# Kernel tuning notes

Measured on AMD Instinct MI355X. Metric: run time of the kernel, lower is better.

The kernel has to match this reference:

```python
import jax, jax.numpy as jnp
import numpy as np

B, C, H, W = 4, 512, 64, 64
CQ = C // 8


def setup_inputs() -> dict:
    key = jax.random.key(0)
    ks = jax.random.split(key, 8)
    s = 0.05
    return {
        "x": jax.random.normal(ks[0], (B, C, H, W), dtype=jnp.float32),
        "wq": jax.random.normal(ks[1], (CQ, C), dtype=jnp.float32) * s,
        "bq": jax.random.normal(ks[2], (CQ,), dtype=jnp.float32) * s,
        "wk": jax.random.normal(ks[3], (CQ, C), dtype=jnp.float32) * s,
        "bk": jax.random.normal(ks[4], (CQ,), dtype=jnp.float32) * s,
        "wv": jax.random.normal(ks[5], (C, C), dtype=jnp.float32) * s,
        "bv": jax.random.normal(ks[6], (C,), dtype=jnp.float32) * s,
        "gamma": jax.random.normal(ks[7], (1,), dtype=jnp.float32) * 0.1,
    }


def reference(x, wq, bq, wk, bk, wv, bv, gamma):
    b, c, h, w = x.shape
    f = x.reshape(b, c, h * w)                       # [B, C, N]
    # 1x1 Conv1d == per-position matmul + bias
    q = jnp.einsum("dc,bcn->bdn", wq, f) + bq[:, None]   # [B, C/8, N]
    k = jnp.einsum("dc,bcn->bdn", wk, f) + bk[:, None]   # [B, C/8, N]
    v = jnp.einsum("dc,bcn->bdn", wv, f) + bv[:, None]   # [B, C, N]
    # query_key[b, i, j] = q_i . k_j  ; softmax over axis=1 (query index)
    qk = jnp.einsum("bdi,bdj->bij", q, k)                # [B, N, N]
    attn = jax.nn.softmax(qk, axis=1)
    o = jnp.einsum("bci,bij->bcj", v, attn)              # [B, C, N]
    return gamma * o.reshape(b, c, h, w) + x
```

## Files before the change

kernel.cpp:

```cpp
#include <hip/hip_runtime.h>
#include <hip/hip_bf16.h>

#define NB 4
#define NC 512
#define NN 4096
#define NM 640
#define IB 64
#define NT (NN / IB)
#define LOG2E 1.4426950408889634f

typedef __attribute__((ext_vector_type(8))) short bf16x8;
typedef __attribute__((ext_vector_type(4))) float f32x4;

__device__ __forceinline__ f32x4 mfma16(bf16x8 a, bf16x8 b, f32x4 c) {
  return __builtin_amdgcn_mfma_f32_16x16x32_bf16(a, b, c, 0, 0, 0);
}

__device__ __forceinline__ unsigned short f2bf(float f) {
  unsigned int u = __float_as_uint(f);
  u += 0x7fffu + ((u >> 16) & 1u);
  return (unsigned short)(u >> 16);
}

typedef const __attribute__((address_space(1))) char gchar_t;
typedef __attribute__((address_space(3))) char lchar_t;

__global__ void pack_w(const float* __restrict__ wq, const float* __restrict__ bq,
                       const float* __restrict__ wk, const float* __restrict__ bk,
                       const float* __restrict__ wv, const float* __restrict__ bv,
                       unsigned short* __restrict__ W, float* __restrict__ bias) {
  int idx = blockIdx.x * 256 + threadIdx.x;
  if (idx < NM * NC) {
    int r = idx >> 9, c = idx & (NC - 1);
    float v;
    if (r < 64) v = wq[r * NC + c];
    else if (r < 128) v = wk[(r - 64) * NC + c];
    else v = wv[(r - 128) * NC + c];
    W[idx] = f2bf(v);
  }
  if (idx < NM)
    bias[idx] = (idx < 64) ? bq[idx] : (idx < 128 ? bk[idx - 64] : bv[idx - 128]);
}

__global__ void xpose(const float* __restrict__ x, unsigned short* __restrict__ XT) {
  __shared__ float t[64][65];
  int b = blockIdx.z;
  int c0 = blockIdx.y * 64, n0 = blockIdx.x * 64;
  int tid = threadIdx.x;
  int lr = tid >> 4;
  int lc4 = (tid & 15) * 4;
  const float* xb = x + (size_t)b * NC * NN;
#pragma unroll
  for (int i = 0; i < 4; ++i) {
    int c = i * 16 + lr;
    float4 v = *reinterpret_cast<const float4*>(xb + (size_t)(c0 + c) * NN + n0 + lc4);
    t[c][lc4 + 0] = v.x; t[c][lc4 + 1] = v.y; t[c][lc4 + 2] = v.z; t[c][lc4 + 3] = v.w;
  }
  __syncthreads();
  unsigned short* xtb = XT + (size_t)b * NN * NC;
#pragma unroll
  for (int i = 0; i < 4; ++i) {
    int n = i * 16 + lr;
    union { unsigned short h[4]; unsigned long long u; } pk;
#pragma unroll
    for (int e = 0; e < 4; ++e) pk.h[e] = f2bf(t[lc4 + e][n]);
    *reinterpret_cast<unsigned long long*>(xtb + (size_t)(n0 + n) * NC + c0 + lc4) = pk.u;
  }
}

__global__ __launch_bounds__(512) void gemm_qkv(
    const unsigned short* __restrict__ W, const float* __restrict__ bias,
    const unsigned short* __restrict__ XT,
    unsigned short* __restrict__ QT, unsigned short* __restrict__ KT,
    unsigned short* __restrict__ V) {
  int b = blockIdx.z;
  int m0 = blockIdx.y * 80;
  int wave = threadIdx.x >> 6, lane = threadIdx.x & 63;
  int nw = blockIdx.x * 512 + wave * 64;
  int lcol = lane & 15, lkg = lane >> 4;
  const unsigned short* xtb = XT + (size_t)b * NN * NC;
  f32x4 acc[5][4] = {};
  for (int k0 = 0; k0 < NC; k0 += 32) {
    int ko = k0 + lkg * 8;
    bf16x8 afr[5], bfr[4];
#pragma unroll
    for (int i = 0; i < 5; ++i)
      afr[i] = *reinterpret_cast<const bf16x8*>(W + (size_t)(m0 + 16 * i + lcol) * NC + ko);
#pragma unroll
    for (int j = 0; j < 4; ++j)
      bfr[j] = *reinterpret_cast<const bf16x8*>(xtb + (size_t)(nw + 16 * j + lcol) * NC + ko);
#pragma unroll
    for (int i = 0; i < 5; ++i)
#pragma unroll
      for (int j = 0; j < 4; ++j)
        acc[i][j] = mfma16(afr[i], bfr[j], acc[i][j]);
  }
  int rbase = lkg * 4;
#pragma unroll
  for (int i = 0; i < 5; ++i) {
    int mrow = m0 + 16 * i;
    if (mrow < 128) {
      bool isq = mrow < 64;
      unsigned short* T = isq ? (QT + (size_t)b * NN * 64) : (KT + (size_t)b * NN * 64);
      int mb = mrow & 63;
      float sc = isq ? LOG2E : 1.0f;
#pragma unroll
      for (int j = 0; j < 4; ++j) {
        int n = nw + 16 * j + lcol;
        union { unsigned short h[4]; unsigned long long u; } pk;
#pragma unroll
        for (int r = 0; r < 4; ++r)
          pk.h[r] = f2bf((acc[i][j][r] + bias[mrow + rbase + r]) * sc);
        *reinterpret_cast<unsigned long long*>(T + (size_t)n * 64 + mb + rbase) = pk.u;
      }
    } else {
      unsigned short* vb = V + (size_t)b * NC * NN;
#pragma unroll
      for (int r = 0; r < 4; ++r) {
        int m = mrow + rbase + r;
        float bs = bias[m];
        int c = m - 128;
#pragma unroll
        for (int j = 0; j < 4; ++j) {
          int n = nw + 16 * j + lcol;
          vb[(size_t)c * NN + n] = f2bf(acc[i][j][r] + bs);
        }
      }
    }
  }
}

__global__ __launch_bounds__(512, 2) void attn_pv(
    const unsigned short* __restrict__ QT, const unsigned short* __restrict__ KT,
    const unsigned short* __restrict__ V, const float* __restrict__ x,
    const float* __restrict__ gamma, float* __restrict__ out) {
  int bid = blockIdx.x;
  int b = (bid & 7) >> 1;
  int jb = ((bid >> 3) << 1) | (bid & 1);
  int j0 = jb * 64;
  int wave = threadIdx.x >> 6, lane = threadIdx.x & 63;
  int lcol = lane & 15, lkg = lane >> 4;
  int sw = wave >> 1;
  int fnh = wave & 1;

  __shared__ __align__(16) unsigned short vlds[2][512 * IB];
  __shared__ __align__(16) unsigned short plds[2][64 * IB];
  __shared__ float sml[4][16][4];

  const unsigned short* qt = QT + (size_t)b * NN * 64;
  const unsigned short* kt = KT + (size_t)b * NN * 64;
  const unsigned short* vp = V + (size_t)b * NC * NN;

  const int lrow = lane >> 3;
  const int lswz = ((lane & 7) ^ lrow) << 3;
  lchar_t* vbase = (lchar_t*)vlds;

  auto stage = [&](int itv, int buf) {
    int i0 = (itv & (NT - 1)) * IB;
    lchar_t* lb = vbase + (size_t)buf * (512 * IB * 2) + wave * (64 * IB * 2);
#pragma unroll
    for (int q = 0; q < 8; ++q) {
      const unsigned short* gp = vp + (size_t)(wave * 64 + q * 8 + lrow) * NN + i0 + lswz;
      __builtin_amdgcn_global_load_lds((gchar_t*)gp, lb + q * 1024, 16, 0, 0);
    }
  };

  bf16x8 kfr[2][2];
#pragma unroll
  for (int f = 0; f < 2; ++f) {
    int fn = 2 * fnh + f;
#pragma unroll
    for (int ks = 0; ks < 2; ++ks)
      kfr[f][ks] = *reinterpret_cast<const bf16x8*>(
          kt + (size_t)(j0 + 16 * fn + lcol) * 64 + ks * 32 + lkg * 8);
  }

  f32x4 oacc[4][4] = {};
  float l_loc[2] = {0.f, 0.f};

  const int jw0 = 16 * (2 * fnh) + lcol, jw1 = jw0 + 16;
  const int pwoff0 = (jw0 * 128 + sw * 32 + lkg * 8) ^ ((jw0 & 7) << 4);
  const int pwoff1 = (jw1 * 128 + sw * 32 + lkg * 8) ^ ((jw1 & 7) << 4);
  const int pxm = (lcol & 7) << 4;
  const int pk0 = lcol * 128 + ((lkg * 16) ^ (pxm & 0x30)) + (pxm & 0x40);
  const int pk1 = pk0 ^ 64;
  const int vk0 = wave * 8192 + lcol * 128 + ((lkg ^ (lcol & 7)) * 16);
  const int vk1 = vk0 ^ 64;

  const char* Pb[2] = {(const char*)plds, (const char*)plds + 64 * IB * 2};
  const char* Vbs[2] = {(const char*)vlds, (const char*)vlds + 512 * IB * 2};

  stage(0, 0);
  bf16x8 qA[2], qB[2];
  {
    int row = sw * 16 + lcol;
    qA[0] = *reinterpret_cast<const bf16x8*>(qt + (size_t)row * 64 + lkg * 8);
    qA[1] = *reinterpret_cast<const bf16x8*>(qt + (size_t)row * 64 + 32 + lkg * 8);
  }

#define PV_ITER(IT, QC, QN, BUF)                                                  \
  {                                                                               \
    const int it_ = (IT);                                                         \
    stage(it_ + 1, (BUF) ^ 1);                                                    \
    f32x4 s[2] = {};                                                              \
    _Pragma("unroll") for (int ks = 0; ks < 2; ++ks)                              \
      _Pragma("unroll") for (int f = 0; f < 2; ++f)                               \
        s[f] = mfma16(QC[ks], kfr[f][ks], s[f]);                                  \
    {                                                                             \
      int row = ((it_ + 1) & (NT - 1)) * IB + sw * 16 + lcol;                     \
      QN[0] = *reinterpret_cast<const bf16x8*>(qt + (size_t)row * 64 + lkg * 8);  \
      QN[1] = *reinterpret_cast<const bf16x8*>(qt + (size_t)row * 64 + 32 + lkg * 8); \
    }                                                                             \
    char* pb = (char*)Pb[BUF];                                                    \
    {                                                                             \
      float p0 = exp2f(s[0][0]), p1 = exp2f(s[0][1]);                             \
      float p2 = exp2f(s[0][2]), p3 = exp2f(s[0][3]);                             \
      l_loc[0] += (p0 + p1) + (p2 + p3);                                          \
      union { unsigned short h[4]; unsigned long long u; } pk;                    \
      pk.h[0] = f2bf(p0); pk.h[1] = f2bf(p1);                                     \
      pk.h[2] = f2bf(p2); pk.h[3] = f2bf(p3);                                     \
      *reinterpret_cast<unsigned long long*>(pb + pwoff0) = pk.u;                 \
    }                                                                             \
    {                                                                             \
      float p0 = exp2f(s[1][0]), p1 = exp2f(s[1][1]);                             \
      float p2 = exp2f(s[1][2]), p3 = exp2f(s[1][3]);                             \
      l_loc[1] += (p0 + p1) + (p2 + p3);                                          \
      union { unsigned short h[4]; unsigned long long u; } pk;                    \
      pk.h[0] = f2bf(p0); pk.h[1] = f2bf(p1);                                     \
      pk.h[2] = f2bf(p2); pk.h[3] = f2bf(p3);                                     \
      *reinterpret_cast<unsigned long long*>(pb + pwoff1) = pk.u;                 \
    }                                                                             \
    asm volatile("s_waitcnt vmcnt(10) lgkmcnt(0)" ::: "memory");                  \
    __builtin_amdgcn_s_barrier();                                                 \
    asm volatile("" ::: "memory");                                                \
    const char* vbw = Vbs[BUF];                                                   \
    __builtin_amdgcn_s_setprio(1);                                                \
    _Pragma("unroll") for (int ks = 0; ks < 2; ++ks) {                            \
      const int pko = ks ? pk1 : pk0;                                             \
      const int vko = ks ? vk1 : vk0;                                             \
      bf16x8 pfr[4];                                                              \
      _Pragma("unroll") for (int fn = 0; fn < 4; ++fn)                            \
        pfr[fn] = *reinterpret_cast<const bf16x8*>(pb + pko + fn * 2048);         \
      _Pragma("unroll") for (int cm = 0; cm < 4; ++cm) {                          \
        bf16x8 vfr = *reinterpret_cast<const bf16x8*>(vbw + vko + cm * 2048);     \
        _Pragma("unroll") for (int fn = 0; fn < 4; ++fn)                          \
          oacc[cm][fn] = mfma16(vfr, pfr[fn], oacc[cm][fn]);                      \
      }                                                                           \
    }                                                                             \
    __builtin_amdgcn_s_setprio(0);                                                \
  }

  for (int it2 = 0; it2 < NT; it2 += 2) {
    PV_ITER(it2 + 0, qA, qB, 0);
    PV_ITER(it2 + 1, qB, qA, 1);
  }
#undef PV_ITER

#pragma unroll
  for (int f = 0; f < 2; ++f) {
    l_loc[f] += __shfl_xor(l_loc[f], 16);
    l_loc[f] += __shfl_xor(l_loc[f], 32);
  }
  if (lane < 16) {
#pragma unroll
    for (int f = 0; f < 2; ++f) sml[2 * fnh + f][lane][sw] = l_loc[f];
  }
  __syncthreads();
  float lj[4];
#pragma unroll
  for (int fn = 0; fn < 4; ++fn) {
    const float* p = sml[fn][lcol];
    lj[fn] = (p[0] + p[1]) + (p[2] + p[3]);
  }

  float g = gamma[0];
  const float* xb = x + (size_t)b * NC * NN;
  float* ob = out + (size_t)b * NC * NN;
#pragma unroll
  for (int fn = 0; fn < 4; ++fn) {
    float sc = g / lj[fn];
    int j = j0 + 16 * fn + lcol;
#pragma unroll
    for (int cm = 0; cm < 4; ++cm) {
      int c = 64 * wave + 16 * cm + lkg * 4;
#pragma unroll
      for (int r = 0; r < 4; ++r) {
        size_t idx = (size_t)(c + r) * NN + j;
        ob[idx] = oacc[cm][fn][r] * sc + xb[idx];
      }
    }
  }
}

extern "C" void kernel_launch(void* const* d_in, const int* in_sizes, int n_in,
                              void* d_out, int out_size, void* d_ws, size_t ws_size,
                              hipStream_t stream) {
  const float* x  = (const float*)d_in[0];
  const float* wq = (const float*)d_in[1];
  const float* bq = (const float*)d_in[2];
  const float* wk = (const float*)d_in[3];
  const float* bk = (const float*)d_in[4];
  const float* wv = (const float*)d_in[5];
  const float* bv = (const float*)d_in[6];
  const float* gm = (const float*)d_in[7];
  float* out = (float*)d_out;

  char* ws = (char*)d_ws;
  unsigned short* XT = (unsigned short*)(ws);
  unsigned short* Vb = (unsigned short*)(ws + (size_t)16 * 1024 * 1024);
  unsigned short* QT = (unsigned short*)(ws + (size_t)32 * 1024 * 1024);
  unsigned short* KT = (unsigned short*)(ws + (size_t)34 * 1024 * 1024);
  unsigned short* Wp = (unsigned short*)(ws + (size_t)36 * 1024 * 1024);
  float* biasp = (float*)(ws + (size_t)36 * 1024 * 1024 + 704 * 1024);

  pack_w<<<(NM * NC + 255) / 256, 256, 0, stream>>>(wq, bq, wk, bk, wv, bv, Wp, biasp);
  xpose<<<dim3(NN / 64, NC / 64, NB), 256, 0, stream>>>(x, XT);
  gemm_qkv<<<dim3(NN / 512, NM / 80, NB), 512, 0, stream>>>(Wp, biasp, XT, QT, KT, Vb);
  attn_pv<<<256, 512, 0, stream>>>(QT, KT, Vb, x, gm, out);
}
```

Measured before the change: 154.2 us.

## Split attention-PV blocks across channel halves with 4-wave blocks and staggered start

The attention-PV kernel changes from 256 blocks of 8 waves to 512 blocks of 4 waves. Each block now covers one half of the 512 channels for a 64-column j tile, and each wave computes all 4 score fragments. The trade is that the QK scores and exp are recomputed twice, once per channel half, in exchange for more blocks and half the V staging LDS per block. Odd j-tiles also start their i-loop halfway around to spread V reads over different addresses.

```diff
diff --git a/kernel.cpp b/kernel.cpp
--- a/kernel.cpp
+++ b/kernel.cpp
@@ -130,22 +130,22 @@
   }
 }
 
-__global__ __launch_bounds__(512, 2) void attn_pv(
+__global__ __launch_bounds__(256, 2) void attn_pv(
     const unsigned short* __restrict__ QT, const unsigned short* __restrict__ KT,
     const unsigned short* __restrict__ V, const float* __restrict__ x,
     const float* __restrict__ gamma, float* __restrict__ out) {
   int bid = blockIdx.x;
-  int b = (bid & 7) >> 1;
-  int jb = ((bid >> 3) << 1) | (bid & 1);
+  int b  = (bid & 7) >> 1;
+  int ch = bid & 1;
+  int jb = bid >> 3;
   int j0 = jb * 64;
+  int st = (jb & 1) * (NT / 2);
   int wave = threadIdx.x >> 6, lane = threadIdx.x & 63;
   int lcol = lane & 15, lkg = lane >> 4;
-  int sw = wave >> 1;
-  int fnh = wave & 1;
-
-  __shared__ __align__(16) unsigned short vlds[2][512 * IB];
+  int sw = wave;
+
+  __shared__ __align__(16) unsigned short vlds[2][256 * IB];
   __shared__ __align__(16) unsigned short plds[2][64 * IB];
-  __shared__ float sml[4][16][4];
 
   const unsigned short* qt = QT + (size_t)b * NN * 64;
   const unsigned short* kt = KT + (size_t)b * NN * 64;
@@ -155,45 +155,44 @@
   const int lswz = ((lane & 7) ^ lrow) << 3;
   lchar_t* vbase = (lchar_t*)vlds;
 
-  auto stage = [&](int itv, int buf) {
-    int i0 = (itv & (NT - 1)) * IB;
-    lchar_t* lb = vbase + (size_t)buf * (512 * IB * 2) + wave * (64 * IB * 2);
+  auto stage = [&](int ite, int buf) {
+    int i0 = ite * IB;
+    lchar_t* lb = vbase + (size_t)buf * (256 * IB * 2) + wave * (64 * IB * 2);
 #pragma unroll
     for (int q = 0; q < 8; ++q) {
-      const unsigned short* gp = vp + (size_t)(wave * 64 + q * 8 + lrow) * NN + i0 + lswz;
+      const unsigned short* gp =
+          vp + (size_t)(ch * 256 + wave * 64 + q * 8 + lrow) * NN + i0 + lswz;
       __builtin_amdgcn_global_load_lds((gchar_t*)gp, lb + q * 1024, 16, 0, 0);
     }
   };
 
-  bf16x8 kfr[2][2];
-#pragma unroll
-  for (int f = 0; f < 2; ++f) {
-    int fn = 2 * fnh + f;
+  bf16x8 kfr[4][2];
+#pragma unroll
+  for (int fn = 0; fn < 4; ++fn)
 #pragma unroll
     for (int ks = 0; ks < 2; ++ks)
-      kfr[f][ks] = *reinterpret_cast<const bf16x8*>(
+      kfr[fn][ks] = *reinterpret_cast<const bf16x8*>(
           kt + (size_t)(j0 + 16 * fn + lcol) * 64 + ks * 32 + lkg * 8);
-  }
 
   f32x4 oacc[4][4] = {};
-  float l_loc[2] = {0.f, 0.f};
-
-  const int jw0 = 16 * (2 * fnh) + lcol, jw1 = jw0 + 16;
-  const int pwoff0 = (jw0 * 128 + sw * 32 + lkg * 8) ^ ((jw0 & 7) << 4);
-  const int pwoff1 = (jw1 * 128 + sw * 32 + lkg * 8) ^ ((jw1 & 7) << 4);
+  float l_loc[4] = {};
+
+  int pwoff[4];
+#pragma unroll
+  for (int fn = 0; fn < 4; ++fn) {
+    int j = 16 * fn + lcol;
+    pwoff[fn] = (j * 128 + sw * 32 + lkg * 8) ^ ((j & 7) << 4);
+  }
   const int pxm = (lcol & 7) << 4;
   const int pk0 = lcol * 128 + ((lkg * 16) ^ (pxm & 0x30)) + (pxm & 0x40);
   const int pk1 = pk0 ^ 64;
   const int vk0 = wave * 8192 + lcol * 128 + ((lkg ^ (lcol & 7)) * 16);
   const int vk1 = vk0 ^ 64;
 
-  const char* Pb[2] = {(const char*)plds, (const char*)plds + 64 * IB * 2};
-  const char* Vbs[2] = {(const char*)vlds, (const char*)vlds + 512 * IB * 2};
-
-  stage(0, 0);
+  stage(st, 0);
   bf16x8 qA[2], qB[2];
   {
-    int row = sw * 16 + lcol;
+    int row = st * IB + sw * 16 + lcol;
     qA[0] = *reinterpret_cast<const bf16x8*>(qt + (size_t)row * 64 + lkg * 8);
     qA[1] = *reinterpret_cast<const bf16x8*>(qt + (size_t)row * 64 + 32 + lkg * 8);
   }
@@ -201,39 +200,31 @@
 #define PV_ITER(IT, QC, QN, BUF)                                                  \
   {                                                                               \
     const int it_ = (IT);                                                         \
-    stage(it_ + 1, (BUF) ^ 1);                                                    \
-    f32x4 s[2] = {};                                                              \
+    const int itn = (it_ + 1 + st) & (NT - 1);                                    \
+    stage(itn, (BUF) ^ 1);                                                        \
+    f32x4 s[4] = {};                                                              \
     _Pragma("unroll") for (int ks = 0; ks < 2; ++ks)                              \
-      _Pragma("unroll") for (int f = 0; f < 2; ++f)                               \
-        s[f] = mfma16(QC[ks], kfr[f][ks], s[f]);                                  \
+      _Pragma("unroll") for (int fn = 0; fn < 4; ++fn)                            \
+        s[fn] = mfma16(QC[ks], kfr[fn][ks], s[fn]);                               \
     {                                                                             \
-      int row = ((it_ + 1) & (NT - 1)) * IB + sw * 16 + lcol;                     \
+      int row = itn * IB + sw * 16 + lcol;                                        \
       QN[0] = *reinterpret_cast<const bf16x8*>(qt + (size_t)row * 64 + lkg * 8);  \
       QN[1] = *reinterpret_cast<const bf16x8*>(qt + (size_t)row * 64 + 32 + lkg * 8); \
     }                                                                             \
-    char* pb = (char*)Pb[BUF];                                                    \
-    {                                                                             \
-      float p0 = exp2f(s[0][0]), p1 = exp2f(s[0][1]);                             \
-      float p2 = exp2f(s[0][2]), p3 = exp2f(s[0][3]);                             \
-      l_loc[0] += (p0 + p1) + (p2 + p3);                                          \
+    char* pb = (char*)plds + (BUF) * (64 * IB * 2);                               \
+    _Pragma("unroll") for (int fn = 0; fn < 4; ++fn) {                            \
+      float p0 = exp2f(s[fn][0]), p1 = exp2f(s[fn][1]);                           \
+      float p2 = exp2f(s[fn][2]), p3 = exp2f(s[fn][3]);                           \
+      l_loc[fn] += (p0 + p1) + (p2 + p3);                                         \
       union { unsigned short h[4]; unsigned long long u; } pk;                    \
       pk.h[0] = f2bf(p0); pk.h[1] = f2bf(p1);                                     \
       pk.h[2] = f2bf(p2); pk.h[3] = f2bf(p3);                                     \
-      *reinterpret_cast<unsigned long long*>(pb + pwoff0) = pk.u;                 \
-    }                                                                             \
-    {                                                                             \
-      float p0 = exp2f(s[1][0]), p1 = exp2f(s[1][1]);                             \
-      float p2 = exp2f(s[1][2]), p3 = exp2f(s[1][3]);                             \
-      l_loc[1] += (p0 + p1) + (p2 + p3);                                          \
-      union { unsigned short h[4]; unsigned long long u; } pk;                    \
-      pk.h[0] = f2bf(p0); pk.h[1] = f2bf(p1);                                     \
-      pk.h[2] = f2bf(p2); pk.h[3] = f2bf(p3);                                     \
-      *reinterpret_cast<unsigned long long*>(pb + pwoff1) = pk.u;                 \
+      *reinterpret_cast<unsigned long long*>(pb + pwoff[fn]) = pk.u;              \
     }                                                                             \
     asm volatile("s_waitcnt vmcnt(10) lgkmcnt(0)" ::: "memory");                  \
     __builtin_amdgcn_s_barrier();                                                 \
     asm volatile("" ::: "memory");                                                \
-    const char* vbw = Vbs[BUF];                                                   \
+    const char* vbw = (const char*)vlds + (BUF) * (256 * IB * 2);                 \
     __builtin_amdgcn_s_setprio(1);                                                \
     _Pragma("unroll") for (int ks = 0; ks < 2; ++ks) {                            \
       const int pko = ks ? pk1 : pk0;                                             \
@@ -250,26 +241,27 @@
     __builtin_amdgcn_s_setprio(0);                                                \
   }
 
-  for (int it2 = 0; it2 < NT; it2 += 2) {
-    PV_ITER(it2 + 0, qA, qB, 0);
-    PV_ITER(it2 + 1, qB, qA, 1);
+  for (int t2 = 0; t2 < NT; t2 += 2) {
+    PV_ITER(t2 + 0, qA, qB, 0);
+    PV_ITER(t2 + 1, qB, qA, 1);
   }
 #undef PV_ITER
 
 #pragma unroll
-  for (int f = 0; f < 2; ++f) {
-    l_loc[f] += __shfl_xor(l_loc[f], 16);
-    l_loc[f] += __shfl_xor(l_loc[f], 32);
-  }
+  for (int fn = 0; fn < 4; ++fn) {
+    l_loc[fn] += __shfl_xor(l_loc[fn], 16);
+    l_loc[fn] += __shfl_xor(l_loc[fn], 32);
+  }
+  float* sml = (float*)plds;
   if (lane < 16) {
 #pragma unroll
-    for (int f = 0; f < 2; ++f) sml[2 * fnh + f][lane][sw] = l_loc[f];
+    for (int fn = 0; fn < 4; ++fn) sml[(fn * 16 + lane) * 4 + sw] = l_loc[fn];
   }
   __syncthreads();
   float lj[4];
 #pragma unroll
   for (int fn = 0; fn < 4; ++fn) {
-    const float* p = sml[fn][lcol];
+    const float* p = &sml[(fn * 16 + lcol) * 4];
     lj[fn] = (p[0] + p[1]) + (p[2] + p[3]);
   }
 
@@ -282,7 +274,7 @@
     int j = j0 + 16 * fn + lcol;
 #pragma unroll
     for (int cm = 0; cm < 4; ++cm) {
-      int c = 64 * wave + 16 * cm + lkg * 4;
+      int c = ch * 256 + wave * 64 + 16 * cm + lkg * 4;
 #pragma unroll
       for (int r = 0; r < 4; ++r) {
         size_t idx = (size_t)(c + r) * NN + j;
@@ -316,5 +308,5 @@
   pack_w<<<(NM * NC + 255) / 256, 256, 0, stream>>>(wq, bq, wk, bk, wv, bv, Wp, biasp);
   xpose<<<dim3(NN / 64, NC / 64, NB), 256, 0, stream>>>(x, XT);
   gemm_qkv<<<dim3(NN / 512, NM / 80, NB), 512, 0, stream>>>(Wp, biasp, XT, QT, KT, Vb);
-  attn_pv<<<256, 512, 0, stream>>>(QT, KT, Vb, x, gm, out);
-}
+  attn_pv<<<512, 256, 0, stream>>>(QT, KT, Vb, x, gm, out);
+}
```

Result: slower. 163.9 us (+6.3%).
